# Performance work log

Measured on AMD Instinct MI355X. Metric: run time of the kernel, lower is better.

The kernel has to match this reference:

```python
import jax, jax.numpy as jnp
import numpy as np
from jax import lax

B, N, C = 4, 1024, 384
H, G, K = 6, 2, 10
GD = C // G   # group dim = 192
HD = C // H   # head dim = 64
SCALE = HD ** -0.5
LN_EPS = 1e-5


def _sqdist(a, b):
    # a: [..., M, 3], b: [..., N, 3] -> squared euclid dist [..., M, N]
    return (jnp.sum(a * a, -1)[..., :, None]
            - 2.0 * jnp.einsum('...mc,...nc->...mn', a, b)
            + jnp.sum(b * b, -1)[..., None, :])


def _layernorm(x, g, b):
    mu = jnp.mean(x, -1, keepdims=True)
    var = jnp.mean(jnp.square(x - mu), -1, keepdims=True)
    return (x - mu) * lax.rsqrt(var + LN_EPS) * g + b


def _forward(q, q_pos, Wq, Wk, Wv, Wvoff, W1, b1, ln_g, ln_b, W2, Wproj, bproj):
    # self-attention path: v = q, v_pos = q_pos
    bidx = jnp.arange(B)[:, None, None]
    # KNN over positions: idx [B, N, K]
    d = _sqdist(q_pos, q_pos)
    _, idx = lax.top_k(-d, K)
    qp = q @ Wq                       # [B, N, C]
    v_off = q @ Wvoff                 # [B, N, C]
    local_v = v_off[bidx, idx]        # [B, N, K, C]
    # split channels into groups: 'b n k (g c) -> b g n k c'
    off_local_v = local_v.reshape(B, N, K, G, GD).transpose(0, 3, 1, 2, 4)
    group_q = qp.reshape(B, N, G, GD).transpose(0, 2, 1, 3)      # [B, G, N, GD]
    shift_feat = jnp.concatenate(
        [off_local_v, jnp.broadcast_to(group_q[:, :, :, None, :], (B, G, N, K, GD))], -1)
    h = _layernorm(shift_feat @ W1 + b1, ln_g, ln_b)
    h = jax.nn.gelu(h, approximate=False)
    offset = jnp.tanh(h @ W2)                                    # [B, G, N, K, 3]
    local_v_pos = q_pos[bidx, idx]                               # [B, N, K, 3]
    shift_pos = (local_v_pos[:, None] + offset).reshape(B, G, N * K, 3)
    # three_nn: 3 nearest v_pos points for each shifted point (squared dists, as in CUDA kernel)
    v_pos_g = jnp.broadcast_to(q_pos[:, None], (B, G, N, 3))
    d2 = _sqdist(shift_pos, v_pos_g)                             # [B, G, N*K, N]
    neg_d3, idx3 = lax.top_k(-d2, 3)
    dist3 = -neg_d3                                              # ascending
    rec = 1.0 / (dist3 + 1e-8)
    w = rec / jnp.sum(rec, -1, keepdims=True)                    # [B, G, N*K, 3]
    # three_interpolate on grouped v features
    v_g = q.reshape(B, N, G, GD).transpose(0, 2, 1, 3)           # [B, G, N, GD]
    gathered = v_g[jnp.arange(B)[:, None, None, None],
                   jnp.arange(G)[None, :, None, None], idx3]      # [B, G, N*K, 3, GD]
    interp = jnp.sum(w[..., None] * gathered, 3)                 # [B, G, N*K, GD]
    # '(b g) (n k) c -> b n k (g c)'
    interp = interp.reshape(B, G, N, K, GD).transpose(0, 2, 3, 1, 4).reshape(B, N, K, C)
    # local cross attention: 1 query vs K keys per token per head
    kk = (interp @ Wk).reshape(B, N, K, H, HD)
    vv = (interp @ Wv).reshape(B, N, K, H, HD)
    qh = qp.reshape(B, N, H, HD)
    attn = jnp.einsum('bnhd,bnkhd->bnhk', qh, kk) * SCALE
    attn = jax.nn.softmax(attn, -1)
    out = jnp.einsum('bnhk,bnkhd->bnhd', attn, vv).reshape(B, N, C)
    return out @ Wproj + bproj


def setup_inputs() -> dict:
    key = jax.random.key(0)
    ks = jax.random.split(key, 12)
    s = 0.02
    return {
        'q': jax.random.normal(ks[0], (B, N, C), jnp.float32),
        'q_pos': jax.random.normal(ks[1], (B, N, 3), jnp.float32),
        'Wq': s * jax.random.normal(ks[2], (C, C), jnp.float32),
        'Wk': s * jax.random.normal(ks[3], (C, C), jnp.float32),
        'Wv': s * jax.random.normal(ks[4], (C, C), jnp.float32),
        'Wvoff': s * jax.random.normal(ks[5], (C, C), jnp.float32),
        'W1': s * jax.random.normal(ks[6], (2 * GD, C), jnp.float32),
        'b1': jnp.zeros((C,), jnp.float32),
        'ln_g': jnp.ones((C,), jnp.float32),
        'ln_b': jnp.zeros((C,), jnp.float32),
        'W2': s * jax.random.normal(ks[7], (C, 3), jnp.float32),
        'Wproj': s * jax.random.normal(ks[8], (C, C), jnp.float32),
        'bproj': jnp.zeros((C,), jnp.float32),
    }


def reference(q, q_pos, Wq, Wk, Wv, Wvoff, W1, b1, ln_g, ln_b, W2, Wproj, bproj):
    return _forward(q, q_pos, Wq, Wk, Wv, Wvoff, W1, b1, ln_g, ln_b, W2, Wproj, bproj)
```

## Files before the change

kernel.cpp:

```cpp
#include <hip/hip_runtime.h>
#include <math.h>

constexpr int B_ = 4;
constexpr int N_ = 1024;
constexpr int C_ = 384;
constexpr int G_ = 2;
constexpr int K_ = 10;
constexpr int GD_ = 192;
constexpr int NK_ = N_ * K_;
constexpr int M2_ = B_ * G_ * N_ * K_;
constexpr float SCALE_ = 0.125f;
constexpr float MARGIN_ = 4e-4f;

__device__ __forceinline__ bool lless(double da, int ia, double db, int ib) {
  return (da < db) || (da == db && ia < ib);
}
__device__ __forceinline__ void lmin2(double& rd, int& ri, double ad, int ai,
                                      double bd, int bi) {
  bool t = lless(bd, bi, ad, ai);
  rd = t ? bd : ad; ri = t ? bi : ai;
}
__device__ __forceinline__ void lmax2(double& rd, int& ri, double ad, int ai,
                                      double bd, int bi) {
  bool t = lless(ad, ai, bd, bi);
  rd = t ? bd : ad; ri = t ? bi : ai;
}
__device__ __forceinline__ void pmin2(float& rd, int& ri, float ad, int ai,
                                      float bd, int bi) {
  bool t = bd < ad;
  rd = t ? bd : ad; ri = t ? bi : ai;
}
__device__ __forceinline__ void pmax2(float& rd, int& ri, float ad, int ai,
                                      float bd, int bi) {
  bool t = ad < bd;
  rd = t ? bd : ad; ri = t ? bi : ai;
}

__global__ void k_zero(int* __restrict__ cnt) { cnt[0] = 0; }

__global__ void k_prep0(const float* __restrict__ q_pos, double* __restrict__ s64,
                        float4* __restrict__ pos4) {
  int i = blockIdx.x * blockDim.x + threadIdx.x;
  if (i >= B_ * N_) return;
  float x = q_pos[3 * i], y = q_pos[3 * i + 1], z = q_pos[3 * i + 2];
  double v = (double)x * x + (double)y * y + (double)z * z;
  s64[i] = v;
  pos4[i] = make_float4(x, y, z, (float)v);
}

__global__ __launch_bounds__(256) void k_knn10_w(const float* __restrict__ q_pos,
                                                 const double* __restrict__ s,
                                                 int* __restrict__ idx10) {
  int wid = (blockIdx.x * blockDim.x + threadIdx.x) >> 6;
  int lane = threadIdx.x & 63;
  if (wid >= B_ * N_) return;
  int b = wid / N_;
  double px = q_pos[3 * wid], py = q_pos[3 * wid + 1], pz = q_pos[3 * wid + 2];
  double sm = s[wid];
  const float* bp = q_pos + b * N_ * 3;
  const double* bs = s + b * N_;
  double d[K_]; int ix[K_];
  #pragma unroll
  for (int j = 0; j < K_; j++) { d[j] = INFINITY; ix[j] = 0x7fffffff; }
  for (int n0 = 0; n0 < N_; n0 += 64) {
    int n = n0 + lane;
    double dot = px * (double)bp[3 * n] + py * (double)bp[3 * n + 1] +
                 pz * (double)bp[3 * n + 2];
    double v = (sm - 2.0 * dot) + bs[n];
    bool c[K_];
    #pragma unroll
    for (int j = 0; j < K_; j++) c[j] = lless(v, n, d[j], ix[j]);
    #pragma unroll
    for (int j = K_ - 1; j >= 1; j--) {
      d[j]  = c[j] ? (c[j - 1] ? d[j - 1] : v) : d[j];
      ix[j] = c[j] ? (c[j - 1] ? ix[j - 1] : n) : ix[j];
    }
    d[0]  = c[0] ? v : d[0];
    ix[0] = c[0] ? n : ix[0];
  }
  #pragma unroll
  for (int off = 1; off < 64; off <<= 1) {
    double bd[K_]; int bi[K_];
    #pragma unroll
    for (int j = 0; j < K_; j++) {
      bd[j] = __shfl_xor(d[j], off);
      bi[j] = __shfl_xor(ix[j], off);
    }
    double md[K_]; int mi[K_];
    #pragma unroll
    for (int r = 0; r < K_; r++) {
      double m; int mj;
      lmin2(m, mj, d[r], ix[r], bd[r], bi[r]);
      #pragma unroll
      for (int j = 1; j <= r; j++) {
        double t; int ti;
        lmax2(t, ti, d[j - 1], ix[j - 1], bd[r - j], bi[r - j]);
        lmin2(m, mj, m, mj, t, ti);
      }
      md[r] = m; mi[r] = mj;
    }
    #pragma unroll
    for (int j = 0; j < K_; j++) { d[j] = md[j]; ix[j] = mi[j]; }
  }
  if (lane == 0) {
    #pragma unroll
    for (int j = 0; j < K_; j++) idx10[wid * K_ + j] = ix[j];
  }
}

template <int TM>
__global__ __launch_bounds__(384) void k_gemmSA(const float* __restrict__ A,
                                                const float* __restrict__ W,
                                                const float* __restrict__ bias,
                                                float* __restrict__ out, int M) {
  int c = threadIdx.x;
  int r0 = blockIdx.x * TM;
  float acc[TM];
  #pragma unroll
  for (int r = 0; r < TM; r++) acc[r] = 0.f;
  #pragma unroll 4
  for (int j = 0; j < C_; j++) {
    float w = W[j * C_ + c];
    #pragma unroll
    for (int r = 0; r < TM; r++) acc[r] = fmaf(A[(r0 + r) * C_ + j], w, acc[r]);
  }
  float bv = bias ? bias[c] : 0.f;
  #pragma unroll
  for (int r = 0; r < TM; r++) out[(r0 + r) * C_ + c] = acc[r] + bv;
}

__global__ __launch_bounds__(384) void k_prepM(const float* __restrict__ Wvoff,
                                               const float* __restrict__ Wq,
                                               const float* __restrict__ W1,
                                               float* __restrict__ M1f,
                                               float* __restrict__ M2f) {
  int g = blockIdx.x / C_;
  int k = blockIdx.x % C_;
  int c = threadIdx.x;
  const float* wv = Wvoff + k * C_ + g * GD_;
  const float* wq = Wq + k * C_ + g * GD_;
  double a1 = 0.0, a2 = 0.0;
  for (int d = 0; d < GD_; d++) {
    a1 += (double)wv[d] * (double)W1[d * C_ + c];
    a2 += (double)wq[d] * (double)W1[(GD_ + d) * C_ + c];
  }
  M1f[(g * C_ + k) * C_ + c] = (float)a1;
  M2f[(g * C_ + k) * C_ + c] = (float)a2;
}

template <int TM>
__global__ __launch_bounds__(384) void k_Y32(const float* __restrict__ q,
                                             const float* __restrict__ M1f,
                                             const float* __restrict__ M2f,
                                             float* __restrict__ Y1f,
                                             float* __restrict__ Y2f) {
  int c = threadIdx.x;
  int g = blockIdx.y;
  int r0 = blockIdx.x * TM;
  float a1[TM], a2[TM];
  #pragma unroll
  for (int r = 0; r < TM; r++) { a1[r] = 0.f; a2[r] = 0.f; }
  const float* m1 = M1f + (size_t)(g * C_) * C_ + c;
  const float* m2 = M2f + (size_t)(g * C_) * C_ + c;
  for (int k = 0; k < C_; k++) {
    float v1 = m1[(size_t)k * C_];
    float v2 = m2[(size_t)k * C_];
    #pragma unroll
    for (int r = 0; r < TM; r++) {
      float av = q[(r0 + r) * C_ + k];
      a1[r] = fmaf(av, v1, a1[r]);
      a2[r] = fmaf(av, v2, a2[r]);
    }
  }
  #pragma unroll
  for (int r = 0; r < TM; r++) {
    Y1f[((size_t)(r0 + r) * G_ + g) * C_ + c] = a1[r];
    Y2f[((size_t)(r0 + r) * G_ + g) * C_ + c] = a2[r];
  }
}

__global__ __launch_bounds__(256) void k_mlptop4(const float* __restrict__ Y1f,
                                                 const float* __restrict__ Y2f,
                                                 const int* __restrict__ idx10,
                                                 const float* __restrict__ q_pos,
                                                 const float* __restrict__ b1,
                                                 const float* __restrict__ ln_g,
                                                 const float* __restrict__ ln_b,
                                                 const float* __restrict__ W2,
                                                 const float4* __restrict__ pos4,
                                                 const float* __restrict__ q,
                                                 float* __restrict__ interp,
                                                 int* __restrict__ flags,
                                                 int* __restrict__ cnt) {
  int w_ = threadIdx.x >> 6, l = threadIdx.x & 63;
  int row = blockIdx.x * 4 + w_;
  int k = row % K_; int t = row / K_;
  int n = t % N_; t /= N_;
  int g = t % G_; int b = t / G_;
  int j = idx10[(b * N_ + n) * K_ + k];
  const float* y1 = Y1f + ((size_t)(b * N_ + j) * G_ + g) * C_;
  const float* y2 = Y2f + ((size_t)(b * N_ + n) * G_ + g) * C_;
  float x[6];
  #pragma unroll
  for (int jj = 0; jj < 6; jj++) {
    int col = l + 64 * jj;
    x[jj] = y1[col] + y2[col] + b1[col];
  }
  float sum = ((((x[0] + x[1]) + x[2]) + x[3]) + x[4]) + x[5];
  #pragma unroll
  for (int off = 1; off < 64; off <<= 1) sum += __shfl_xor(sum, off);
  float mu = sum * (1.0f / 384.0f);
  float sq = 0.f;
  #pragma unroll
  for (int jj = 0; jj < 6; jj++) { float dd = x[jj] - mu; sq = fmaf(dd, dd, sq); }
  #pragma unroll
  for (int off = 1; off < 64; off <<= 1) sq += __shfl_xor(sq, off);
  float var = sq * (1.0f / 384.0f);
  float rstd = 1.0f / sqrtf(var + 1e-5f);
  float ge[6];
  #pragma unroll
  for (int jj = 0; jj < 6; jj++) {
    int col = l + 64 * jj;
    float nv = (x[jj] - mu) * rstd * ln_g[col] + ln_b[col];
    ge[jj] = 0.5f * nv * (1.0f + erff(nv * 0.70710678118654752f));
  }
  float o3[3];
  #pragma unroll
  for (int o = 0; o < 3; o++) {
    float p = 0.f;
    #pragma unroll
    for (int jj = 0; jj < 6; jj++) {
      int col = l + 64 * jj;
      p = fmaf(ge[jj], W2[col * 3 + o], p);
    }
    #pragma unroll
    for (int off = 1; off < 64; off <<= 1) p += __shfl_xor(p, off);
    o3[o] = tanhf(p);
  }
  int gi = b * N_ + j;
  float px = q_pos[gi * 3 + 0] + o3[0];
  float py = q_pos[gi * 3 + 1] + o3[1];
  float pz = q_pos[gi * 3 + 2] + o3[2];
  float sp = fmaf(px, px, fmaf(py, py, pz * pz));
  float nx = -2.0f * px, ny = -2.0f * py, nz = -2.0f * pz;
  const float4* p4 = pos4 + b * N_;
  float d[4]; int ix[4];
  #pragma unroll
  for (int jj = 0; jj < 4; jj++) { d[jj] = INFINITY; ix[jj] = 0x7fffffff; }
  for (int n0 = 0; n0 < N_; n0 += 64) {
    int nn = n0 + l;
    float4 pv = p4[nn];
    float v = fmaf(nx, pv.x, fmaf(ny, pv.y, fmaf(nz, pv.z, sp + pv.w)));
    bool c0 = v < d[0], c1 = v < d[1], c2 = v < d[2], c3 = v < d[3];
    d[3]  = c3 ? (c2 ? d[2] : v) : d[3];
    ix[3] = c3 ? (c2 ? ix[2] : nn) : ix[3];
    d[2]  = c2 ? (c1 ? d[1] : v) : d[2];
    ix[2] = c2 ? (c1 ? ix[1] : nn) : ix[2];
    d[1]  = c1 ? (c0 ? d[0] : v) : d[1];
    ix[1] = c1 ? (c0 ? ix[0] : nn) : ix[1];
    d[0]  = c0 ? v : d[0];
    ix[0] = c0 ? nn : ix[0];
  }
  #pragma unroll
  for (int off = 1; off < 64; off <<= 1) {
    float bd[4]; int bi[4];
    #pragma unroll
    for (int jj = 0; jj < 4; jj++) {
      bd[jj] = __shfl_xor(d[jj], off);
      bi[jj] = __shfl_xor(ix[jj], off);
    }
    float md[4]; int mi[4];
    #pragma unroll
    for (int r = 0; r < 4; r++) {
      float mm; int mj;
      pmin2(mm, mj, d[r], ix[r], bd[r], bi[r]);
      #pragma unroll
      for (int jj = 1; jj <= r; jj++) {
        float tt; int ti;
        pmax2(tt, ti, d[jj - 1], ix[jj - 1], bd[r - jj], bi[r - jj]);
        pmin2(mm, mj, mm, mj, tt, ti);
      }
      md[r] = mm; mi[r] = mj;
    }
    #pragma unroll
    for (int jj = 0; jj < 4; jj++) { d[jj] = md[jj]; ix[jj] = mi[jj]; }
  }
  if (d[3] - d[2] < MARGIN_) {
    if (l == 0) {
      int pos = atomicAdd(cnt, 1);
      flags[pos] = row;
    }
    return;
  }
  float r0 = 1.0f / (d[0] + 1e-8f);
  float r1 = 1.0f / (d[1] + 1e-8f);
  float r2 = 1.0f / (d[2] + 1e-8f);
  float rs = (r0 + r1) + r2;
  float w0 = r0 / rs, w1 = r1 / rs, w2 = r2 / rs;
  const float* qb = q + (size_t)b * N_ * C_ + g * GD_;
  const float* p0 = qb + (size_t)ix[0] * C_;
  const float* p1 = qb + (size_t)ix[1] * C_;
  const float* p2 = qb + (size_t)ix[2] * C_;
  float* op = interp + (((size_t)(b * N_ + n) * K_ + k) * C_) + g * GD_;
  #pragma unroll
  for (int cc0 = 0; cc0 < GD_; cc0 += 64) {
    int cc = cc0 + l;
    op[cc] = (w0 * p0[cc] + w1 * p1[cc]) + w2 * p2[cc];
  }
}

__global__ __launch_bounds__(256) void k_fix(const int* __restrict__ cnt,
                                             const int* __restrict__ flags,
                                             const float* __restrict__ q,
                                             const float* __restrict__ Wvoff,
                                             const float* __restrict__ Wq,
                                             const float* __restrict__ W1,
                                             const int* __restrict__ idx10,
                                             const float* __restrict__ q_pos,
                                             const double* __restrict__ s64,
                                             const float* __restrict__ b1,
                                             const float* __restrict__ ln_g,
                                             const float* __restrict__ ln_b,
                                             const float* __restrict__ W2,
                                             float* __restrict__ interp) {
  __shared__ double vbuf[4][2][GD_];
  int w_ = threadIdx.x >> 6;
  int gwid = blockIdx.x * 4 + w_;
  int lane = threadIdx.x & 63;
  int nwaves = gridDim.x * 4;
  int total = cnt[0];
  for (int i = gwid; i < total; i += nwaves) {
    int wid = __builtin_amdgcn_readfirstlane(flags[i]);
    int m = wid % NK_; int t = wid / NK_;
    int g = t % G_; int b = t / G_;
    int n_ = m / K_, k_ = m % K_;
    int j = __builtin_amdgcn_readfirstlane(idx10[(b * N_ + n_) * K_ + k_]);
    const float* qj = q + (size_t)(b * N_ + j) * C_;
    const float* qn = q + (size_t)(b * N_ + n_) * C_;
    const float* wvo = Wvoff + g * GD_;
    const float* wqg = Wq + g * GD_;
    double a0 = 0.0, a1 = 0.0, a2 = 0.0, b0 = 0.0, b1a = 0.0, b2 = 0.0;
    for (int tt = 0; tt < C_; tt++) {
      double qjt = (double)qj[tt];
      double qnt = (double)qn[tt];
      const float* r1 = wvo + (size_t)tt * C_;
      const float* r2 = wqg + (size_t)tt * C_;
      a0 += qjt * (double)r1[lane];
      a1 += qjt * (double)r1[lane + 64];
      a2 += qjt * (double)r1[lane + 128];
      b0 += qnt * (double)r2[lane];
      b1a += qnt * (double)r2[lane + 64];
      b2 += qnt * (double)r2[lane + 128];
    }
    vbuf[w_][0][lane] = a0; vbuf[w_][0][lane + 64] = a1; vbuf[w_][0][lane + 128] = a2;
    vbuf[w_][1][lane] = b0; vbuf[w_][1][lane + 64] = b1a; vbuf[w_][1][lane + 128] = b2;
    double x[6];
    #pragma unroll
    for (int jj = 0; jj < 6; jj++) x[jj] = 0.0;
    for (int d = 0; d < GD_; d++) {
      double v1d = vbuf[w_][0][d];
      double v2d = vbuf[w_][1][d];
      const float* w1t = W1 + (size_t)d * C_;
      const float* w1b = W1 + (size_t)(GD_ + d) * C_;
      #pragma unroll
      for (int jj = 0; jj < 6; jj++) {
        int col = lane + 64 * jj;
        x[jj] += v1d * (double)w1t[col] + v2d * (double)w1b[col];
      }
    }
    #pragma unroll
    for (int jj = 0; jj < 6; jj++) x[jj] += (double)b1[lane + 64 * jj];
    double sum = ((((x[0] + x[1]) + x[2]) + x[3]) + x[4]) + x[5];
    #pragma unroll
    for (int off = 1; off < 64; off <<= 1) sum += __shfl_xor(sum, off);
    double mu = sum / 384.0;
    double sq = 0.0;
    #pragma unroll
    for (int jj = 0; jj < 6; jj++) { double dd = x[jj] - mu; sq += dd * dd; }
    #pragma unroll
    for (int off = 1; off < 64; off <<= 1) sq += __shfl_xor(sq, off);
    double var = sq / 384.0;
    double rstd = 1.0 / sqrt(var + 1e-5);
    double ge[6];
    #pragma unroll
    for (int jj = 0; jj < 6; jj++) {
      int col = lane + 64 * jj;
      double nv = (x[jj] - mu) * rstd * (double)ln_g[col] + (double)ln_b[col];
      ge[jj] = 0.5 * nv * (1.0 + erf(nv * 0.70710678118654752440));
    }
    double o3[3];
    #pragma unroll
    for (int o = 0; o < 3; o++) {
      double p = 0.0;
      #pragma unroll
      for (int jj = 0; jj < 6; jj++) {
        int col = lane + 64 * jj;
        p += ge[jj] * (double)W2[col * 3 + o];
      }
      #pragma unroll
      for (int off = 1; off < 64; off <<= 1) p += __shfl_xor(p, off);
      o3[o] = tanh(p);
    }
    int gi = b * N_ + j;
    double px = (double)q_pos[gi * 3 + 0] + o3[0];
    double py = (double)q_pos[gi * 3 + 1] + o3[1];
    double pz = (double)q_pos[gi * 3 + 2] + o3[2];
    double sp = px * px + py * py + pz * pz;
    const float* bp = q_pos + b * N_ * 3;
    const double* bs = s64 + b * N_;
    double d0 = INFINITY, d1 = INFINITY, d2 = INFINITY;
    int i0 = 0x7fffffff, i1 = 0x7fffffff, i2 = 0x7fffffff;
    for (int n = lane; n < N_; n += 64) {
      double dot = px * (double)bp[3 * n] + py * (double)bp[3 * n + 1] +
                   pz * (double)bp[3 * n + 2];
      double dd = (sp - 2.0 * dot) + bs[n];
      bool c0 = lless(dd, n, d0, i0);
      bool c1 = lless(dd, n, d1, i1);
      bool c2 = lless(dd, n, d2, i2);
      double nd2 = c2 ? (c1 ? d1 : dd) : d2; int ni2 = c2 ? (c1 ? i1 : n) : i2;
      double nd1 = c1 ? (c0 ? d0 : dd) : d1; int ni1 = c1 ? (c0 ? i0 : n) : i1;
      double nd0 = c0 ? dd : d0;             int ni0 = c0 ? n : i0;
      d0 = nd0; d1 = nd1; d2 = nd2; i0 = ni0; i1 = ni1; i2 = ni2;
    }
    #pragma unroll
    for (int off = 1; off < 64; off <<= 1) {
      double e0 = __shfl_xor(d0, off), e1 = __shfl_xor(d1, off), e2 = __shfl_xor(d2, off);
      int j0 = __shfl_xor(i0, off), j1 = __shfl_xor(i1, off), j2 = __shfl_xor(i2, off);
      double mnd, mxd, p1d, q1d, q2d, q3d, q4d, t1d, t2d;
      int mni, mxi, p1i, q1i, q2i, q3i, q4i, t1i, t2i;
      lmin2(mnd, mni, d0, i0, e0, j0);
      lmax2(mxd, mxi, d0, i0, e0, j0);
      lmin2(p1d, p1i, d1, i1, e1, j1);
      lmin2(t1d, t1i, p1d, p1i, mxd, mxi);
      lmax2(q1d, q1i, d1, i1, e0, j0);
      lmax2(q2d, q2i, d0, i0, e1, j1);
      lmin2(q3d, q3i, q1d, q1i, q2d, q2i);
      lmin2(q4d, q4i, d2, i2, e2, j2);
      lmin2(t2d, t2i, q3d, q3i, q4d, q4i);
      d0 = mnd; i0 = mni; d1 = t1d; i1 = t1i; d2 = t2d; i2 = t2i;
    }
    double r0 = 1.0 / (d0 + 1e-8);
    double r1 = 1.0 / (d1 + 1e-8);
    double r2 = 1.0 / (d2 + 1e-8);
    double rs = (r0 + r1) + r2;
    float w0 = (float)(r0 / rs), w1 = (float)(r1 / rs), w2 = (float)(r2 / rs);
    const float* qb = q + (size_t)b * N_ * C_ + g * GD_;
    const float* p0 = qb + (size_t)i0 * C_;
    const float* p1 = qb + (size_t)i1 * C_;
    const float* p2 = qb + (size_t)i2 * C_;
    float* op = interp + (((size_t)(b * N_ + n_) * K_ + k_) * C_) + g * GD_;
    #pragma unroll
    for (int cc0 = 0; cc0 < GD_; cc0 += 64) {
      int cc = cc0 + lane;
      op[cc] = (w0 * p0[cc] + w1 * p1[cc]) + w2 * p2[cc];
    }
  }
}

__global__ __launch_bounds__(256) void k_T(const float* __restrict__ Wk,
                                           float* __restrict__ WkT) {
  int i = blockIdx.x * blockDim.x + threadIdx.x;
  if (i >= C_ * C_) return;
  int r = i / C_, c = i % C_;
  WkT[c * C_ + r] = Wk[i];
}

template <int TM>
__global__ __launch_bounds__(384) void k_U(const float* __restrict__ qp,
                                           const float* __restrict__ WkT,
                                           float* __restrict__ U) {
  int c = threadIdx.x;
  int r0 = blockIdx.x * TM;
  for (int h = 0; h < 6; h++) {
    float acc[TM];
    #pragma unroll
    for (int r = 0; r < TM; r++) acc[r] = 0.f;
    #pragma unroll 4
    for (int dd = 0; dd < 64; dd++) {
      float w = WkT[(h * 64 + dd) * C_ + c];
      #pragma unroll
      for (int r = 0; r < TM; r++)
        acc[r] = fmaf(qp[(r0 + r) * C_ + h * 64 + dd], w, acc[r]);
    }
    #pragma unroll
    for (int r = 0; r < TM; r++) U[((size_t)(r0 + r) * 6 + h) * C_ + c] = acc[r];
  }
}

__global__ __launch_bounds__(256) void k_attn2(const float* __restrict__ interp,
                                               float* __restrict__ Umix) {
  int wid = blockIdx.x * 4 + (threadIdx.x >> 6);
  int lane = threadIdx.x & 63;
  int bn = wid / 6;
  float* urow = Umix + (size_t)wid * C_;
  float u[6];
  #pragma unroll
  for (int j = 0; j < 6; j++) u[j] = urow[lane + 64 * j];
  float logit[K_];
  #pragma unroll
  for (int k = 0; k < K_; k++) {
    const float* ip = interp + ((size_t)bn * K_ + k) * C_;
    float p = 0.f;
    #pragma unroll
    for (int j = 0; j < 6; j++) p = fmaf(ip[lane + 64 * j], u[j], p);
    #pragma unroll
    for (int off = 1; off < 64; off <<= 1) p += __shfl_xor(p, off);
    logit[k] = p * SCALE_;
  }
  float mx = logit[0];
  #pragma unroll
  for (int k = 1; k < K_; k++) mx = fmaxf(mx, logit[k]);
  float e[K_], se = 0.f;
  #pragma unroll
  for (int k = 0; k < K_; k++) { e[k] = expf(logit[k] - mx); se += e[k]; }
  float inv = 1.0f / se;
  #pragma unroll
  for (int k = 0; k < K_; k++) e[k] *= inv;
  #pragma unroll
  for (int j = 0; j < 6; j++) {
    float mv = 0.f;
    #pragma unroll
    for (int k = 0; k < K_; k++)
      mv = fmaf(e[k], interp[((size_t)bn * K_ + k) * C_ + lane + 64 * j], mv);
    urow[lane + 64 * j] = mv;
  }
}

template <int TM>
__global__ __launch_bounds__(384) void k_out(const float* __restrict__ mix,
                                             const float* __restrict__ Wv,
                                             float* __restrict__ attn_out) {
  int c = threadIdx.x;
  int h = __builtin_amdgcn_readfirstlane(threadIdx.x) >> 6;
  int r0 = blockIdx.x * TM;
  float acc[TM];
  #pragma unroll
  for (int r = 0; r < TM; r++) acc[r] = 0.f;
  #pragma unroll 4
  for (int ci = 0; ci < C_; ci++) {
    float w = Wv[ci * C_ + c];
    #pragma unroll
    for (int r = 0; r < TM; r++)
      acc[r] = fmaf(mix[((size_t)(r0 + r) * 6 + h) * C_ + ci], w, acc[r]);
  }
  #pragma unroll
  for (int r = 0; r < TM; r++) attn_out[(size_t)(r0 + r) * C_ + c] = acc[r];
}

extern "C" void kernel_launch(void* const* d_in, const int* in_sizes, int n_in,
                              void* d_out, int out_size, void* d_ws, size_t ws_size,
                              hipStream_t stream) {
  const float* q     = (const float*)d_in[0];
  const float* q_pos = (const float*)d_in[1];
  const float* Wq    = (const float*)d_in[2];
  const float* Wk    = (const float*)d_in[3];
  const float* Wv    = (const float*)d_in[4];
  const float* Wvoff = (const float*)d_in[5];
  const float* W1    = (const float*)d_in[6];
  const float* b1    = (const float*)d_in[7];
  const float* ln_g  = (const float*)d_in[8];
  const float* ln_b  = (const float*)d_in[9];
  const float* W2    = (const float*)d_in[10];
  const float* Wproj = (const float*)d_in[11];
  const float* bproj = (const float*)d_in[12];
  float* out = (float*)d_out;

  char* ws = (char*)d_ws;
  char* U0 = ws; ws += 38 * 1024 * 1024;
  float*  Y1f    = (float*)(U0);
  float*  Y2f    = (float*)(U0 + 12582912);
  float*  M1f    = (float*)(U0 + 25165824);
  float*  M2f    = (float*)(U0 + 26345472);
  int*    idx10  = (int*)  (U0 + 28508160);
  int*    flags  = (int*)  (U0 + 28672000);
  float4* pos4   = (float4*)(U0 + 28999680);
  int*    cnt    = (int*)  (U0 + 29065216);
  float*  Umix   = (float*)U0;
  double* s64    = (double*)ws; ws += (size_t)B_ * N_ * 8;
  float*  qp32   = (float*)ws;  ws += (size_t)B_ * N_ * C_ * 4;
  float*  interp = (float*)ws;  ws += (size_t)B_ * N_ * K_ * C_ * 4;
  float*  WkT    = (float*)ws;  ws += (size_t)C_ * C_ * 4;
  float*  attn_out = qp32;

  k_zero<<<1, 1, 0, stream>>>(cnt);
  k_prep0<<<(B_ * N_ + 255) / 256, 256, 0, stream>>>(q_pos, s64, pos4);
  k_knn10_w<<<B_ * N_ / 4, 256, 0, stream>>>(q_pos, s64, idx10);
  k_gemmSA<8><<<B_ * N_ / 8, 384, 0, stream>>>(q, Wq, nullptr, qp32, B_ * N_);
  k_prepM<<<G_ * C_, 384, 0, stream>>>(Wvoff, Wq, W1, M1f, M2f);
  k_Y32<8><<<dim3(B_ * N_ / 8, G_), 384, 0, stream>>>(q, M1f, M2f, Y1f, Y2f);
  k_mlptop4<<<M2_ / 4, 256, 0, stream>>>(Y1f, Y2f, idx10, q_pos, b1, ln_g, ln_b,
                                         W2, pos4, q, interp, flags, cnt);
  k_fix<<<512, 256, 0, stream>>>(cnt, flags, q, Wvoff, Wq, W1, idx10, q_pos, s64,
                                 b1, ln_g, ln_b, W2, interp);
  k_T<<<(C_ * C_ + 255) / 256, 256, 0, stream>>>(Wk, WkT);
  k_U<8><<<B_ * N_ / 8, 384, 0, stream>>>(qp32, WkT, Umix);
  k_attn2<<<B_ * N_ * 6 / 4, 256, 0, stream>>>(interp, Umix);
  k_out<8><<<B_ * N_ / 8, 384, 0, stream>>>(Umix, Wv, attn_out);
  k_gemmSA<8><<<B_ * N_ / 8, 384, 0, stream>>>(attn_out, Wproj, bproj, out, B_ * N_);
}
```

Baseline: 660.1 us.

## Fold small kernels into neighbours, simplify top-4 merge, cache interp in registers

Result: faster. 646.0 us (-2.1%).

```diff
diff --git a/kernel.cpp b/kernel.cpp
--- a/kernel.cpp
+++ b/kernel.cpp
@@ -36,11 +36,10 @@
   rd = t ? bd : ad; ri = t ? bi : ai;
 }
 
-__global__ void k_zero(int* __restrict__ cnt) { cnt[0] = 0; }
-
 __global__ void k_prep0(const float* __restrict__ q_pos, double* __restrict__ s64,
-                        float4* __restrict__ pos4) {
+                        float4* __restrict__ pos4, int* __restrict__ cnt) {
   int i = blockIdx.x * blockDim.x + threadIdx.x;
+  if (i == 0) cnt[0] = 0;
   if (i >= B_ * N_) return;
   float x = q_pos[3 * i], y = q_pos[3 * i + 1], z = q_pos[3 * i + 2];
   double v = (double)x * x + (double)y * y + (double)z * z;
@@ -132,11 +131,14 @@
 __global__ __launch_bounds__(384) void k_prepM(const float* __restrict__ Wvoff,
                                                const float* __restrict__ Wq,
                                                const float* __restrict__ W1,
+                                               const float* __restrict__ Wk,
                                                float* __restrict__ M1f,
-                                               float* __restrict__ M2f) {
+                                               float* __restrict__ M2f,
+                                               float* __restrict__ WkT) {
   int g = blockIdx.x / C_;
   int k = blockIdx.x % C_;
   int c = threadIdx.x;
+  if (g == 0) WkT[c * C_ + k] = Wk[k * C_ + c];
   const float* wv = Wvoff + k * C_ + g * GD_;
   const float* wq = Wq + k * C_ + g * GD_;
   double a1 = 0.0, a2 = 0.0;
@@ -244,63 +246,58 @@
   float sp = fmaf(px, px, fmaf(py, py, pz * pz));
   float nx = -2.0f * px, ny = -2.0f * py, nz = -2.0f * pz;
   const float4* p4 = pos4 + b * N_;
-  float d[4]; int ix[4];
-  #pragma unroll
-  for (int jj = 0; jj < 4; jj++) { d[jj] = INFINITY; ix[jj] = 0x7fffffff; }
+  float d0 = INFINITY, d1 = INFINITY, d2 = INFINITY, r4 = INFINITY;
+  int i0 = 0x7fffffff, i1 = 0x7fffffff, i2 = 0x7fffffff;
   for (int n0 = 0; n0 < N_; n0 += 64) {
     int nn = n0 + l;
     float4 pv = p4[nn];
     float v = fmaf(nx, pv.x, fmaf(ny, pv.y, fmaf(nz, pv.z, sp + pv.w)));
-    bool c0 = v < d[0], c1 = v < d[1], c2 = v < d[2], c3 = v < d[3];
-    d[3]  = c3 ? (c2 ? d[2] : v) : d[3];
-    ix[3] = c3 ? (c2 ? ix[2] : nn) : ix[3];
-    d[2]  = c2 ? (c1 ? d[1] : v) : d[2];
-    ix[2] = c2 ? (c1 ? ix[1] : nn) : ix[2];
-    d[1]  = c1 ? (c0 ? d[0] : v) : d[1];
-    ix[1] = c1 ? (c0 ? ix[0] : nn) : ix[1];
-    d[0]  = c0 ? v : d[0];
-    ix[0] = c0 ? nn : ix[0];
+    bool c0 = v < d0, c1 = v < d1, c2 = v < d2;
+    float disp = c2 ? d2 : v;
+    r4 = fminf(r4, disp);
+    d2 = c2 ? (c1 ? d1 : v) : d2;
+    i2 = c2 ? (c1 ? i1 : nn) : i2;
+    d1 = c1 ? (c0 ? d0 : v) : d1;
+    i1 = c1 ? (c0 ? i0 : nn) : i1;
+    d0 = c0 ? v : d0;
+    i0 = c0 ? nn : i0;
   }
   #pragma unroll
   for (int off = 1; off < 64; off <<= 1) {
-    float bd[4]; int bi[4];
-    #pragma unroll
-    for (int jj = 0; jj < 4; jj++) {
-      bd[jj] = __shfl_xor(d[jj], off);
-      bi[jj] = __shfl_xor(ix[jj], off);
-    }
-    float md[4]; int mi[4];
-    #pragma unroll
-    for (int r = 0; r < 4; r++) {
-      float mm; int mj;
-      pmin2(mm, mj, d[r], ix[r], bd[r], bi[r]);
-      #pragma unroll
-      for (int jj = 1; jj <= r; jj++) {
-        float tt; int ti;
-        pmax2(tt, ti, d[jj - 1], ix[jj - 1], bd[r - jj], bi[r - jj]);
-        pmin2(mm, mj, mm, mj, tt, ti);
-      }
-      md[r] = mm; mi[r] = mj;
-    }
-    #pragma unroll
-    for (int jj = 0; jj < 4; jj++) { d[jj] = md[jj]; ix[jj] = mi[jj]; }
-  }
-  if (d[3] - d[2] < MARGIN_) {
+    float e0 = __shfl_xor(d0, off), e1 = __shfl_xor(d1, off), e2 = __shfl_xor(d2, off);
+    float er = __shfl_xor(r4, off);
+    int j0 = __shfl_xor(i0, off), j1 = __shfl_xor(i1, off), j2 = __shfl_xor(i2, off);
+    float va = fmaxf(d0, e2), vb = fmaxf(d1, e1), vc = fmaxf(d2, e0);
+    float r4n = fminf(fminf(r4, er), fminf(fminf(va, vb), vc));
+    float m0d, t1d, u1d, m1d, t2a, t2b, u2d, w2d, m2d;
+    int m0i, t1i, u1i, m1i, t2ai, t2bi, u2i, w2i, m2i;
+    pmin2(m0d, m0i, d0, i0, e0, j0);
+    pmax2(t1d, t1i, d0, i0, e0, j0);
+    pmin2(u1d, u1i, d1, i1, e1, j1);
+    pmin2(m1d, m1i, u1d, u1i, t1d, t1i);
+    pmax2(t2a, t2ai, d1, i1, e0, j0);
+    pmax2(t2b, t2bi, d0, i0, e1, j1);
+    pmin2(u2d, u2i, d2, i2, e2, j2);
+    pmin2(w2d, w2i, t2a, t2ai, t2b, t2bi);
+    pmin2(m2d, m2i, u2d, u2i, w2d, w2i);
+    d0 = m0d; i0 = m0i; d1 = m1d; i1 = m1i; d2 = m2d; i2 = m2i; r4 = r4n;
+  }
+  if (r4 - d2 < MARGIN_) {
     if (l == 0) {
       int pos = atomicAdd(cnt, 1);
       flags[pos] = row;
     }
     return;
   }
-  float r0 = 1.0f / (d[0] + 1e-8f);
-  float r1 = 1.0f / (d[1] + 1e-8f);
-  float r2 = 1.0f / (d[2] + 1e-8f);
+  float r0 = 1.0f / (d0 + 1e-8f);
+  float r1 = 1.0f / (d1 + 1e-8f);
+  float r2 = 1.0f / (d2 + 1e-8f);
   float rs = (r0 + r1) + r2;
   float w0 = r0 / rs, w1 = r1 / rs, w2 = r2 / rs;
   const float* qb = q + (size_t)b * N_ * C_ + g * GD_;
-  const float* p0 = qb + (size_t)ix[0] * C_;
-  const float* p1 = qb + (size_t)ix[1] * C_;
-  const float* p2 = qb + (size_t)ix[2] * C_;
+  const float* p0 = qb + (size_t)i0 * C_;
+  const float* p1 = qb + (size_t)i1 * C_;
+  const float* p2 = qb + (size_t)i2 * C_;
   float* op = interp + (((size_t)(b * N_ + n) * K_ + k) * C_) + g * GD_;
   #pragma unroll
   for (int cc0 = 0; cc0 < GD_; cc0 += 64) {
@@ -457,14 +454,6 @@
   }
 }
 
-__global__ __launch_bounds__(256) void k_T(const float* __restrict__ Wk,
-                                           float* __restrict__ WkT) {
-  int i = blockIdx.x * blockDim.x + threadIdx.x;
-  if (i >= C_ * C_) return;
-  int r = i / C_, c = i % C_;
-  WkT[c * C_ + r] = Wk[i];
-}
-
 template <int TM>
 __global__ __launch_bounds__(384) void k_U(const float* __restrict__ qp,
                                            const float* __restrict__ WkT,
@@ -496,13 +485,17 @@
   float u[6];
   #pragma unroll
   for (int j = 0; j < 6; j++) u[j] = urow[lane + 64 * j];
+  float ipv[K_][6];
   float logit[K_];
   #pragma unroll
   for (int k = 0; k < K_; k++) {
     const float* ip = interp + ((size_t)bn * K_ + k) * C_;
     float p = 0.f;
     #pragma unroll
-    for (int j = 0; j < 6; j++) p = fmaf(ip[lane + 64 * j], u[j], p);
+    for (int j = 0; j < 6; j++) {
+      ipv[k][j] = ip[lane + 64 * j];
+      p = fmaf(ipv[k][j], u[j], p);
+    }
     #pragma unroll
     for (int off = 1; off < 64; off <<= 1) p += __shfl_xor(p, off);
     logit[k] = p * SCALE_;
@@ -520,8 +513,7 @@
   for (int j = 0; j < 6; j++) {
     float mv = 0.f;
     #pragma unroll
-    for (int k = 0; k < K_; k++)
-      mv = fmaf(e[k], interp[((size_t)bn * K_ + k) * C_ + lane + 64 * j], mv);
+    for (int k = 0; k < K_; k++) mv = fmaf(e[k], ipv[k][j], mv);
     urow[lane + 64 * j] = mv;
   }
 }
@@ -582,17 +574,15 @@
   float*  WkT    = (float*)ws;  ws += (size_t)C_ * C_ * 4;
   float*  attn_out = qp32;
 
-  k_zero<<<1, 1, 0, stream>>>(cnt);
-  k_prep0<<<(B_ * N_ + 255) / 256, 256, 0, stream>>>(q_pos, s64, pos4);
+  k_prep0<<<(B_ * N_ + 255) / 256, 256, 0, stream>>>(q_pos, s64, pos4, cnt);
   k_knn10_w<<<B_ * N_ / 4, 256, 0, stream>>>(q_pos, s64, idx10);
   k_gemmSA<8><<<B_ * N_ / 8, 384, 0, stream>>>(q, Wq, nullptr, qp32, B_ * N_);
-  k_prepM<<<G_ * C_, 384, 0, stream>>>(Wvoff, Wq, W1, M1f, M2f);
+  k_prepM<<<G_ * C_, 384, 0, stream>>>(Wvoff, Wq, W1, Wk, M1f, M2f, WkT);
   k_Y32<8><<<dim3(B_ * N_ / 8, G_), 384, 0, stream>>>(q, M1f, M2f, Y1f, Y2f);
   k_mlptop4<<<M2_ / 4, 256, 0, stream>>>(Y1f, Y2f, idx10, q_pos, b1, ln_g, ln_b,
                                          W2, pos4, q, interp, flags, cnt);
   k_fix<<<512, 256, 0, stream>>>(cnt, flags, q, Wvoff, Wq, W1, idx10, q_pos, s64,
                                  b1, ln_g, ln_b, W2, interp);
-  k_T<<<(C_ * C_ + 255) / 256, 256, 0, stream>>>(Wk, WkT);
   k_U<8><<<B_ * N_ / 8, 384, 0, stream>>>(qp32, WkT, Umix);
   k_attn2<<<B_ * N_ * 6 / 4, 256, 0, stream>>>(interp, Umix);
   k_out<8><<<B_ * N_ / 8, 384, 0, stream>>>(Umix, Wv, attn_out);
```
